# Optimization experiments

Hardware: AMD Instinct MI355X
Metric: run time of the kernel (lower is better)

The kernel has to match this reference:

```python
import jax, jax.numpy as jnp
import numpy as np

B, T, D, H = 2, 2048, 1024, 16
HD = D // H  # head_dim = 64

def setup_inputs() -> dict:
    key = jax.random.key(0)
    ks = jax.random.split(key, 5)
    s = 0.02
    return {
        "x": jax.random.normal(ks[0], (B, T, D), dtype=jnp.float32),
        "w_qkv": jax.random.normal(ks[1], (3 * D, D), dtype=jnp.float32) * s,
        "b_qkv": jax.random.normal(ks[2], (3 * D,), dtype=jnp.float32) * s,
        "w_proj": jax.random.normal(ks[3], (D, D), dtype=jnp.float32) * s,
        "b_proj": jax.random.normal(ks[4], (D,), dtype=jnp.float32) * s,
    }

def reference(x, w_qkv, b_qkv, w_proj, b_proj):
    b, t, c = x.shape
    h, hd = H, HD
    scale = hd ** -0.5
    # qkv projection (torch Linear: x @ W^T + b)
    qkv = x @ w_qkv.T + b_qkv                      # [b, t, 3c]
    q, k, v = jnp.split(qkv, 3, axis=-1)
    # b t (h d) -> b h t d
    reshape = lambda z: z.reshape(b, t, h, hd).transpose(0, 2, 1, 3)
    q, k, v = reshape(q), reshape(k), reshape(v)
    scores = jnp.einsum("bhqd,bhkd->bhqk", q, k) * scale  # [b, h, t, t]
    causal = jnp.triu(jnp.ones((t, t), dtype=bool), k=1)   # True above diag
    scores = jnp.where(causal[None, None], -jnp.inf, scores)
    attn = jax.nn.softmax(scores, axis=-1)
    out = jnp.einsum("bhqk,bhkd->bhqd", attn, v)            # [b, h, t, d]
    out = out.transpose(0, 2, 1, 3).reshape(b, t, c)        # b h t d -> b t (h d)
    return out @ w_proj.T + b_proj
```

## Files before the change

kernel.cpp:

```cpp
#include <hip/hip_runtime.h>
#include <hip/hip_bf16.h>

#define Bq 2
#define Tq 2048
#define Dq 1024
#define Hq 16
#define HDq 64

typedef __attribute__((ext_vector_type(8))) short short8;
typedef __attribute__((ext_vector_type(4))) float f32x4;

__device__ __forceinline__ unsigned short f2bf(float f) {
  union { float f; unsigned int i; } v; v.f = f;
  unsigned int r = v.i + 0x7fffu + ((v.i >> 16) & 1u);
  return (unsigned short)(r >> 16);
}

__device__ __forceinline__ short8 cvt8(const float* __restrict__ g) {
  const float4* gp = (const float4*)g;
  float4 x0 = gp[0], x1 = gp[1];
  short8 v;
  v[0] = (short)f2bf(x0.x); v[1] = (short)f2bf(x0.y);
  v[2] = (short)f2bf(x0.z); v[3] = (short)f2bf(x0.w);
  v[4] = (short)f2bf(x1.x); v[5] = (short)f2bf(x1.y);
  v[6] = (short)f2bf(x1.z); v[7] = (short)f2bf(x1.w);
  return v;
}

__device__ __forceinline__ void async_cp16(const void* g, void* l) {
  __builtin_amdgcn_global_load_lds(
      (const __attribute__((address_space(1))) void*)g,
      (__attribute__((address_space(3))) void*)l, 16, 0, 0);
}

constexpr int NXC = (Bq * Tq * Dq) / 8;
constexpr int NW1C = (3 * Dq * Dq) / 8;
constexpr int NW2C = (Dq * Dq) / 8;

__global__ __launch_bounds__(256)
void cvt_all(const float* __restrict__ x, const float* __restrict__ w1,
             const float* __restrict__ w2, unsigned short* __restrict__ xo,
             unsigned short* __restrict__ w1o, unsigned short* __restrict__ w2o)
{
  int i = blockIdx.x * 256 + threadIdx.x;
  const float* src; unsigned short* dst; int j;
  if (i < NXC)              { src = x;  dst = xo;  j = i; }
  else if (i < NXC + NW1C)  { src = w1; dst = w1o; j = i - NXC; }
  else                      { src = w2; dst = w2o; j = i - NXC - NW1C; }
  *(short8*)&dst[(size_t)j * 8] = cvt8(src + (size_t)j * 8);
}

template<int EPI, int BN_>
__global__ __launch_bounds__(256)
void gemm_bt(const unsigned short* __restrict__ Ab, const unsigned short* __restrict__ Wb,
             const float* __restrict__ bias, float* __restrict__ outp,
             int K, int N,
             unsigned short* __restrict__ qo, unsigned short* __restrict__ ko,
             unsigned short* __restrict__ vo)
{
  constexpr int WN = BN_ / 2;
  constexpr int NJ = WN / 16;
  constexpr int NBI = BN_ / 64;
  __shared__ unsigned short As[128 * 32];
  __shared__ unsigned short Bs[BN_ * 32];

  const int t = threadIdx.x;
  const int lane = t & 63, w = t >> 6;
  const int m0 = blockIdx.y * 128, n0 = blockIdx.x * BN_;
  const int fr = lane & 15, qd = lane >> 4;
  const int wm = (w >> 1) * 64, wn = (w & 1) * WN;

  f32x4 acc[4][NJ] = {};

  for (int k0 = 0; k0 < K; k0 += 32) {
    __syncthreads();
    #pragma unroll
    for (int j = 0; j < 2; j++) {
      int G = (2 * w + j) * 64 + lane;
      int row = G >> 2, g = G & 3;
      async_cp16(Ab + (size_t)(m0 + row) * K + k0 + g * 8, &As[G * 8]);
    }
    #pragma unroll
    for (int j = 0; j < NBI; j++) {
      int G = (NBI * w + j) * 64 + lane;
      int row = G >> 2, g = G & 3;
      async_cp16(Wb + (size_t)(n0 + row) * K + k0 + g * 8, &Bs[G * 8]);
    }
    __syncthreads();
    short8 af[4], bf[NJ];
    #pragma unroll
    for (int ib = 0; ib < 4; ib++)
      af[ib] = *(const short8*)&As[(wm + ib * 16 + fr) * 32 + qd * 8];
    #pragma unroll
    for (int jb = 0; jb < NJ; jb++)
      bf[jb] = *(const short8*)&Bs[(wn + jb * 16 + fr) * 32 + qd * 8];
    #pragma unroll
    for (int ib = 0; ib < 4; ib++)
      #pragma unroll
      for (int jb = 0; jb < NJ; jb++)
        acc[ib][jb] = __builtin_amdgcn_mfma_f32_16x16x32_bf16(af[ib], bf[jb], acc[ib][jb], 0, 0, 0);
  }

  #pragma unroll
  for (int jb = 0; jb < NJ; jb++) {
    int col = n0 + wn + jb * 16 + fr;
    float bv = bias[col];
    if (EPI == 0) {
      int which = col >> 10;
      int rem = col & 1023;
      int hh = rem >> 6, dd = rem & 63;
      #pragma unroll
      for (int ib = 0; ib < 4; ib++) {
        int row4 = m0 + wm + ib * 16 + qd * 4;
        int bb = row4 >> 11, tt = row4 & (Tq - 1);
        if (which == 2) {
          unsigned lo = (unsigned)f2bf(acc[ib][jb][0] + bv)
                      | ((unsigned)f2bf(acc[ib][jb][1] + bv) << 16);
          unsigned hi = (unsigned)f2bf(acc[ib][jb][2] + bv)
                      | ((unsigned)f2bf(acc[ib][jb][3] + bv) << 16);
          uint2 pk; pk.x = lo; pk.y = hi;
          *(uint2*)&vo[((size_t)(bb * Hq + hh) * HDq + dd) * Tq + tt] = pk;
        } else {
          unsigned short* dst = (which == 0) ? qo : ko;
          #pragma unroll
          for (int r = 0; r < 4; r++)
            dst[((size_t)(bb * Hq + hh) * Tq + tt + r) * HDq + dd] = f2bf(acc[ib][jb][r] + bv);
        }
      }
    } else {
      #pragma unroll
      for (int ib = 0; ib < 4; ib++)
        #pragma unroll
        for (int r = 0; r < 4; r++) {
          int row = m0 + wm + ib * 16 + qd * 4 + r;
          outp[(size_t)row * N + col] = acc[ib][jb][r] + bv;
        }
    }
  }
}

constexpr int AP = 72;

__global__ __launch_bounds__(256, 1)
void attn_fwd(const unsigned short* __restrict__ qb, const unsigned short* __restrict__ kb,
              const unsigned short* __restrict__ vtb, unsigned short* __restrict__ ab)
{
  __shared__ unsigned short Ks[2][64 * 64];
  __shared__ unsigned short Vts[2][64 * 64];
  __shared__ unsigned short Ps[128 * AP];

  const int t = threadIdx.x, w = t >> 6, lane = t & 63;
  const int fr = lane & 15, qd = lane >> 4;
  const int i = blockIdx.x;
  const int bh = blockIdx.y;
  const int q0t[2] = { (15 - i) * 128, i * 128 };
  const int ktmax = 31 - 2 * i;
  const int ktsmall = 2 * i + 1;

  short8 aq[2][2][2];
  #pragma unroll
  for (int tl = 0; tl < 2; tl++) {
    const unsigned short* Qg = qb + ((size_t)bh * Tq + q0t[tl]) * HDq;
    #pragma unroll
    for (int s = 0; s < 2; s++)
      #pragma unroll
      for (int c = 0; c < 2; c++)
        aq[tl][s][c] = *(const short8*)(Qg + (w * 32 + s * 16 + fr) * 64 + c * 32 + qd * 8);
  }

  const unsigned short* Kbh = kb + (size_t)bh * Tq * HDq;
  const unsigned short* Vbh = vtb + (size_t)bh * HDq * Tq;

  const int off0 = ((qd ^ (fr & 7)) * 8);
  const int off1 = off0 ^ 32;

  float lsum[2][2][4] = {};
  f32x4 oacc[2][2][4] = {};
  const float SCL = 0.125f * 1.44269504088896f;

  const int G0 = 2 * w * 64 + lane, G1 = G0 + 64;
  const int r0 = G0 >> 3, g0 = (G0 & 7) ^ (r0 & 7);
  const int r1 = G1 >> 3, g1 = (G1 & 7) ^ (r1 & 7);

  async_cp16(Kbh + (size_t)r0 * 64 + g0 * 8, &Ks[0][G0 * 8]);
  async_cp16(Vbh + (size_t)r0 * Tq + g0 * 8, &Vts[0][G0 * 8]);
  async_cp16(Kbh + (size_t)r1 * 64 + g1 * 8, &Ks[0][G1 * 8]);
  async_cp16(Vbh + (size_t)r1 * Tq + g1 * 8, &Vts[0][G1 * 8]);

  for (int kt = 0; kt <= ktmax; kt++) {
    const int cur = kt & 1;
    __syncthreads();
    if (kt < ktmax) {
      const int nxt = cur ^ 1;
      const size_t kofs = (size_t)(kt + 1) * 64;
      async_cp16(Kbh + (kofs + r0) * 64 + g0 * 8, &Ks[nxt][G0 * 8]);
      async_cp16(Vbh + (size_t)r0 * Tq + kofs + g0 * 8, &Vts[nxt][G0 * 8]);
      async_cp16(Kbh + (kofs + r1) * 64 + g1 * 8, &Ks[nxt][G1 * 8]);
      async_cp16(Vbh + (size_t)r1 * Tq + kofs + g1 * 8, &Vts[nxt][G1 * 8]);
    }

    short8 bk[4][2], bv[4][2];
    #pragma unroll
    for (int nb = 0; nb < 4; nb++) {
      bk[nb][0] = *(const short8*)&Ks[cur][(nb * 16 + fr) * 64 + off0];
      bk[nb][1] = *(const short8*)&Ks[cur][(nb * 16 + fr) * 64 + off1];
      bv[nb][0] = *(const short8*)&Vts[cur][(nb * 16 + fr) * 64 + off0];
      bv[nb][1] = *(const short8*)&Vts[cur][(nb * 16 + fr) * 64 + off1];
    }

    const int ntiles = (kt <= ktsmall) ? 2 : 1;
    for (int tl = 0; tl < ntiles; tl++) {
      const bool diag = (kt >= 2 * ((tl == 0) ? (15 - i) : i));
      #pragma unroll
      for (int s = 0; s < 2; s++) {
        f32x4 sacc[4] = {};
        #pragma unroll
        for (int nb = 0; nb < 4; nb++) {
          sacc[nb] = __builtin_amdgcn_mfma_f32_16x16x32_bf16(aq[tl][s][0], bk[nb][0], sacc[nb], 0, 0, 0);
          sacc[nb] = __builtin_amdgcn_mfma_f32_16x16x32_bf16(aq[tl][s][1], bk[nb][1], sacc[nb], 0, 0, 0);
        }
        const int qrow = q0t[tl] + w * 32 + s * 16 + qd * 4;
        #pragma unroll
        for (int nb = 0; nb < 4; nb++)
          #pragma unroll
          for (int reg = 0; reg < 4; reg++) {
            float pv = exp2f(sacc[nb][reg] * SCL);
            if (diag && (kt * 64 + nb * 16 + fr) > (qrow + reg)) pv = 0.f;
            lsum[tl][s][reg] += pv;
            Ps[(w * 32 + s * 16 + qd * 4 + reg) * AP + nb * 16 + fr] = f2bf(pv);
          }
        short8 ap0 = *(const short8*)&Ps[(w * 32 + s * 16 + fr) * AP + qd * 8];
        short8 ap1 = *(const short8*)&Ps[(w * 32 + s * 16 + fr) * AP + 32 + qd * 8];
        #pragma unroll
        for (int db = 0; db < 4; db++) {
          oacc[tl][s][db] = __builtin_amdgcn_mfma_f32_16x16x32_bf16(ap0, bv[db][0], oacc[tl][s][db], 0, 0, 0);
          oacc[tl][s][db] = __builtin_amdgcn_mfma_f32_16x16x32_bf16(ap1, bv[db][1], oacc[tl][s][db], 0, 0, 0);
        }
      }
    }
  }

  #pragma unroll
  for (int tl = 0; tl < 2; tl++)
    #pragma unroll
    for (int s = 0; s < 2; s++)
      #pragma unroll
      for (int reg = 0; reg < 4; reg++) {
        float ls = lsum[tl][s][reg];
        ls += __shfl_xor(ls, 1);
        ls += __shfl_xor(ls, 2);
        ls += __shfl_xor(ls, 4);
        ls += __shfl_xor(ls, 8);
        float linv = 1.0f / ls;
        size_t rowoff = ((size_t)(bh >> 4) * Tq + q0t[tl] + w * 32 + s * 16 + qd * 4 + reg) * Dq
                      + (bh & 15) * HDq;
        #pragma unroll
        for (int db = 0; db < 4; db++)
          ab[rowoff + db * 16 + fr] = f2bf(oacc[tl][s][db][reg] * linv);
      }
}

extern "C" void kernel_launch(void* const* d_in, const int* in_sizes, int n_in,
                              void* d_out, int out_size, void* d_ws, size_t ws_size,
                              hipStream_t stream) {
  const float* x      = (const float*)d_in[0];
  const float* w_qkv  = (const float*)d_in[1];
  const float* b_qkv  = (const float*)d_in[2];
  const float* w_proj = (const float*)d_in[3];
  const float* b_proj = (const float*)d_in[4];
  float* out = (float*)d_out;

  unsigned short* ws = (unsigned short*)d_ws;
  const size_t NE = (size_t)Bq * Hq * Tq * HDq;
  unsigned short* qb  = ws;
  unsigned short* kb  = ws + NE;
  unsigned short* vtb = ws + 2 * NE;
  unsigned short* ab  = ws + 3 * NE;
  unsigned short* xb  = ws + 4 * NE;
  unsigned short* wqb = xb + (size_t)NXC * 8;
  unsigned short* wpb = wqb + (size_t)NW1C * 8;

  dim3 blk(256);
  cvt_all<<<dim3((NXC + NW1C + NW2C) >> 8), blk, 0, stream>>>(x, w_qkv, w_proj, xb, wqb, wpb);

  dim3 g1(3 * Dq / 128, Bq * Tq / 128);
  gemm_bt<0, 128><<<g1, blk, 0, stream>>>(xb, wqb, b_qkv, nullptr,
                                          Dq, 3 * Dq, qb, kb, vtb);
  dim3 g2(8, Bq * Hq);
  attn_fwd<<<g2, blk, 0, stream>>>(qb, kb, vtb, ab);
  dim3 g3(Dq / 64, Bq * Tq / 128);
  gemm_bt<1, 64><<<g3, blk, 0, stream>>>(ab, wpb, b_proj, out,
                                         Dq, Dq, nullptr, nullptr, nullptr);
}
```

Baseline: 213.3 us.

## Split attention into 64-row strip pairs, MFMA row sums, two blocks per CU

Reworks the causal attention kernel so each block handles a pair of 64-row query strips (one from the front, one from the back) instead of pairs of 128-row tiles. This doubles the grid to 16x32 blocks and allows two blocks per CU via launch bounds. It also computes softmax row sums with an extra MFMA against a ones vector instead of per-lane adds plus shuffles, and uses a cheaper round-half-up bf16 conversion for P. The risks are a smaller per-wave tile and less K/V reuse per loaded tile, extra MFMA work for the sums, and slightly different rounding.

```diff
diff --git a/kernel.cpp b/kernel.cpp
--- a/kernel.cpp
+++ b/kernel.cpp
@@ -14,6 +14,10 @@
   union { float f; unsigned int i; } v; v.f = f;
   unsigned int r = v.i + 0x7fffu + ((v.i >> 16) & 1u);
   return (unsigned short)(r >> 16);
+}
+__device__ __forceinline__ unsigned short f2bf_fast(float f) {
+  union { float f; unsigned int i; } v; v.f = f;
+  return (unsigned short)((v.i + 0x8000u) >> 16);
 }
 
 __device__ __forceinline__ short8 cvt8(const float* __restrict__ g) {
@@ -141,7 +145,39 @@
 
 constexpr int AP = 72;
 
-__global__ __launch_bounds__(256, 1)
+template<bool DIAG>
+__device__ __forceinline__ void strip_compute(
+    const short8 aq0, const short8 aq1,
+    const short8 (&bk)[4][2], const short8 (&bv)[4][2], const short8 ones,
+    unsigned short* __restrict__ PsRow, int fr, int qd, int qbase,
+    f32x4 (&oacc)[4], f32x4& lacc, float SCL)
+{
+  f32x4 s4[4] = {};
+  #pragma unroll
+  for (int nb = 0; nb < 4; nb++) {
+    s4[nb] = __builtin_amdgcn_mfma_f32_16x16x32_bf16(aq0, bk[nb][0], s4[nb], 0, 0, 0);
+    s4[nb] = __builtin_amdgcn_mfma_f32_16x16x32_bf16(aq1, bk[nb][1], s4[nb], 0, 0, 0);
+  }
+  #pragma unroll
+  for (int nb = 0; nb < 4; nb++)
+    #pragma unroll
+    for (int reg = 0; reg < 4; reg++) {
+      float pv = exp2f(s4[nb][reg] * SCL);
+      if (DIAG && (nb * 16 + fr) > (qbase + reg)) pv = 0.f;
+      PsRow[(qd * 4 + reg) * AP + nb * 16 + fr] = f2bf_fast(pv);
+    }
+  short8 ap0 = *(const short8*)&PsRow[fr * AP + qd * 8];
+  short8 ap1 = *(const short8*)&PsRow[fr * AP + 32 + qd * 8];
+  lacc = __builtin_amdgcn_mfma_f32_16x16x32_bf16(ap0, ones, lacc, 0, 0, 0);
+  lacc = __builtin_amdgcn_mfma_f32_16x16x32_bf16(ap1, ones, lacc, 0, 0, 0);
+  #pragma unroll
+  for (int db = 0; db < 4; db++) {
+    oacc[db] = __builtin_amdgcn_mfma_f32_16x16x32_bf16(ap0, bv[db][0], oacc[db], 0, 0, 0);
+    oacc[db] = __builtin_amdgcn_mfma_f32_16x16x32_bf16(ap1, bv[db][1], oacc[db], 0, 0, 0);
+  }
+}
+
+__global__ __launch_bounds__(256, 2)
 void attn_fwd(const unsigned short* __restrict__ qb, const unsigned short* __restrict__ kb,
               const unsigned short* __restrict__ vtb, unsigned short* __restrict__ ab)
 {
@@ -151,21 +187,21 @@
 
   const int t = threadIdx.x, w = t >> 6, lane = t & 63;
   const int fr = lane & 15, qd = lane >> 4;
-  const int i = blockIdx.x;
+  const int p = blockIdx.x;
   const int bh = blockIdx.y;
-  const int q0t[2] = { (15 - i) * 128, i * 128 };
-  const int ktmax = 31 - 2 * i;
-  const int ktsmall = 2 * i + 1;
-
-  short8 aq[2][2][2];
+  const int sB = 31 - p;
+  const int sA = p;
+  const int s0t[2] = { sB * 64, sA * 64 };
+  const int ktB = sB;
+  const int qbase = w * 16 + qd * 4;
+
+  short8 aq[2][2];
   #pragma unroll
   for (int tl = 0; tl < 2; tl++) {
-    const unsigned short* Qg = qb + ((size_t)bh * Tq + q0t[tl]) * HDq;
-    #pragma unroll
-    for (int s = 0; s < 2; s++)
-      #pragma unroll
-      for (int c = 0; c < 2; c++)
-        aq[tl][s][c] = *(const short8*)(Qg + (w * 32 + s * 16 + fr) * 64 + c * 32 + qd * 8);
+    const unsigned short* Qg = qb + ((size_t)bh * Tq + s0t[tl]) * HDq;
+    #pragma unroll
+    for (int c = 0; c < 2; c++)
+      aq[tl][c] = *(const short8*)(Qg + (w * 16 + fr) * 64 + c * 32 + qd * 8);
   }
 
   const unsigned short* Kbh = kb + (size_t)bh * Tq * HDq;
@@ -173,24 +209,31 @@
 
   const int off0 = ((qd ^ (fr & 7)) * 8);
   const int off1 = off0 ^ 32;
-
-  float lsum[2][2][4] = {};
-  f32x4 oacc[2][2][4] = {};
-  const float SCL = 0.125f * 1.44269504088896f;
 
   const int G0 = 2 * w * 64 + lane, G1 = G0 + 64;
   const int r0 = G0 >> 3, g0 = (G0 & 7) ^ (r0 & 7);
   const int r1 = G1 >> 3, g1 = (G1 & 7) ^ (r1 & 7);
+
+  short8 ones;
+  #pragma unroll
+  for (int j = 0; j < 8; j++) ones[j] = (short)0x3F80;
+
+  f32x4 oacc[2][4] = {};
+  f32x4 lacc[2] = {};
+  const float SCL = 0.125f * 1.44269504088896f;
+
+  unsigned short* PsB = &Ps[(0 * 64 + w * 16) * AP];
+  unsigned short* PsA = &Ps[(1 * 64 + w * 16) * AP];
 
   async_cp16(Kbh + (size_t)r0 * 64 + g0 * 8, &Ks[0][G0 * 8]);
   async_cp16(Vbh + (size_t)r0 * Tq + g0 * 8, &Vts[0][G0 * 8]);
   async_cp16(Kbh + (size_t)r1 * 64 + g1 * 8, &Ks[0][G1 * 8]);
   async_cp16(Vbh + (size_t)r1 * Tq + g1 * 8, &Vts[0][G1 * 8]);
 
-  for (int kt = 0; kt <= ktmax; kt++) {
+  for (int kt = 0; kt <= ktB; kt++) {
     const int cur = kt & 1;
     __syncthreads();
-    if (kt < ktmax) {
+    if (kt < ktB) {
       const int nxt = cur ^ 1;
       const size_t kofs = (size_t)(kt + 1) * 64;
       async_cp16(Kbh + (kofs + r0) * 64 + g0 * 8, &Ks[nxt][G0 * 8]);
@@ -208,56 +251,28 @@
       bv[nb][1] = *(const short8*)&Vts[cur][(nb * 16 + fr) * 64 + off1];
     }
 
-    const int ntiles = (kt <= ktsmall) ? 2 : 1;
-    for (int tl = 0; tl < ntiles; tl++) {
-      const bool diag = (kt >= 2 * ((tl == 0) ? (15 - i) : i));
+    if (kt == ktB)
+      strip_compute<true >(aq[0][0], aq[0][1], bk, bv, ones, PsB, fr, qd, qbase, oacc[0], lacc[0], SCL);
+    else
+      strip_compute<false>(aq[0][0], aq[0][1], bk, bv, ones, PsB, fr, qd, qbase, oacc[0], lacc[0], SCL);
+
+    if (kt < sA)
+      strip_compute<false>(aq[1][0], aq[1][1], bk, bv, ones, PsA, fr, qd, qbase, oacc[1], lacc[1], SCL);
+    else if (kt == sA)
+      strip_compute<true >(aq[1][0], aq[1][1], bk, bv, ones, PsA, fr, qd, qbase, oacc[1], lacc[1], SCL);
+  }
+
+  #pragma unroll
+  for (int tl = 0; tl < 2; tl++)
+    #pragma unroll
+    for (int reg = 0; reg < 4; reg++) {
+      float linv = 1.0f / lacc[tl][reg];
+      size_t rowoff = ((size_t)(bh >> 4) * Tq + s0t[tl] + w * 16 + qd * 4 + reg) * Dq
+                    + (bh & 15) * HDq;
       #pragma unroll
-      for (int s = 0; s < 2; s++) {
-        f32x4 sacc[4] = {};
-        #pragma unroll
-        for (int nb = 0; nb < 4; nb++) {
-          sacc[nb] = __builtin_amdgcn_mfma_f32_16x16x32_bf16(aq[tl][s][0], bk[nb][0], sacc[nb], 0, 0, 0);
-          sacc[nb] = __builtin_amdgcn_mfma_f32_16x16x32_bf16(aq[tl][s][1], bk[nb][1], sacc[nb], 0, 0, 0);
-        }
-        const int qrow = q0t[tl] + w * 32 + s * 16 + qd * 4;
-        #pragma unroll
-        for (int nb = 0; nb < 4; nb++)
-          #pragma unroll
-          for (int reg = 0; reg < 4; reg++) {
-            float pv = exp2f(sacc[nb][reg] * SCL);
-            if (diag && (kt * 64 + nb * 16 + fr) > (qrow + reg)) pv = 0.f;
-            lsum[tl][s][reg] += pv;
-            Ps[(w * 32 + s * 16 + qd * 4 + reg) * AP + nb * 16 + fr] = f2bf(pv);
-          }
-        short8 ap0 = *(const short8*)&Ps[(w * 32 + s * 16 + fr) * AP + qd * 8];
-        short8 ap1 = *(const short8*)&Ps[(w * 32 + s * 16 + fr) * AP + 32 + qd * 8];
-        #pragma unroll
-        for (int db = 0; db < 4; db++) {
-          oacc[tl][s][db] = __builtin_amdgcn_mfma_f32_16x16x32_bf16(ap0, bv[db][0], oacc[tl][s][db], 0, 0, 0);
-          oacc[tl][s][db] = __builtin_amdgcn_mfma_f32_16x16x32_bf16(ap1, bv[db][1], oacc[tl][s][db], 0, 0, 0);
-        }
-      }
-    }
-  }
-
-  #pragma unroll
-  for (int tl = 0; tl < 2; tl++)
-    #pragma unroll
-    for (int s = 0; s < 2; s++)
-      #pragma unroll
-      for (int reg = 0; reg < 4; reg++) {
-        float ls = lsum[tl][s][reg];
-        ls += __shfl_xor(ls, 1);
-        ls += __shfl_xor(ls, 2);
-        ls += __shfl_xor(ls, 4);
-        ls += __shfl_xor(ls, 8);
-        float linv = 1.0f / ls;
-        size_t rowoff = ((size_t)(bh >> 4) * Tq + q0t[tl] + w * 32 + s * 16 + qd * 4 + reg) * Dq
-                      + (bh & 15) * HDq;
-        #pragma unroll
-        for (int db = 0; db < 4; db++)
-          ab[rowoff + db * 16 + fr] = f2bf(oacc[tl][s][db][reg] * linv);
-      }
+      for (int db = 0; db < 4; db++)
+        ab[rowoff + db * 16 + fr] = f2bf(oacc[tl][db][reg] * linv);
+    }
 }
 
 extern "C" void kernel_launch(void* const* d_in, const int* in_sizes, int n_in,
@@ -286,7 +301,7 @@
   dim3 g1(3 * Dq / 128, Bq * Tq / 128);
   gemm_bt<0, 128><<<g1, blk, 0, stream>>>(xb, wqb, b_qkv, nullptr,
                                           Dq, 3 * Dq, qb, kb, vtb);
-  dim3 g2(8, Bq * Hq);
+  dim3 g2(16, Bq * Hq);
   attn_fwd<<<g2, blk, 0, stream>>>(qb, kb, vtb, ab);
   dim3 g3(Dq / 64, Bq * Tq / 128);
   gemm_bt<1, 64><<<g3, blk, 0, stream>>>(ab, wpb, b_proj, out,
```

After: 197.8 us. 7.3% less time.
